# Performance work log

Measured on AMD Instinct MI355X. Metric: run time of the kernel, lower is better.

## Reference

```python
import jax, jax.numpy as jnp
import numpy as np

B, S, HID = 4, 4096, 768
NH, HD = 12, 64
KF = NH * HD          # 768, == HID
TTT_H = 2048
CS = 512              # chunk_size
NC = S // CS
LR = 0.001


def setup_inputs() -> dict:
    key = jax.random.key(0)
    ks = jax.random.split(key, 6)
    std = 0.02
    return {
        "x": jax.random.normal(ks[0], (B, S, HID), dtype=jnp.float32),
        "w_qkv": jax.random.normal(ks[1], (HID, 3 * HID), dtype=jnp.float32) * std,
        "w0": jax.random.normal(ks[2], (KF, TTT_H), dtype=jnp.float32) * std,
        "w1": jax.random.normal(ks[3], (TTT_H, HID), dtype=jnp.float32) * std,
        "w2": jax.random.normal(ks[4], (KF, TTT_H), dtype=jnp.float32) * std,
        "w_out": jax.random.normal(ks[5], (HID, HID), dtype=jnp.float32) * std,
    }


def _fast_forward(w0, w1, w2, k_in):
    # k_in: [B, CS, KF] -> [B, CS, HID]; SwiGLU-style fast-weight MLP
    gate = jax.nn.silu(k_in @ w0)
    hidden = k_in @ w2
    return (gate * hidden) @ w1


def reference(x, w_qkv, w0, w1, w2, w_out):
    qkv = x @ w_qkv                                   # [B,S,3*HID]
    q, k, v = jnp.split(qkv, 3, axis=-1)
    q = q.reshape(B, S, NH, HD)
    k = k.reshape(B, S, NH, HD)
    v = v.reshape(B, S, NH, HD)

    def step(carry, chunk_idx):
        w0c, w1c, w2c = carry
        start = chunk_idx * CS
        kc = jax.lax.dynamic_slice(k, (0, start, 0, 0), (B, CS, NH, HD)).reshape(B, CS, KF)
        vc = jax.lax.dynamic_slice(v, (0, start, 0, 0), (B, CS, NH, HD)).reshape(B, CS, KF)

        def loss_fn(a0, a1, a2):
            v_pred = _fast_forward(a0, a1, a2, kc)
            return jnp.mean((v_pred - vc) ** 2)

        loss, (g0, g1, g2) = jax.value_and_grad(loss_fn, argnums=(0, 1, 2))(w0c, w1c, w2c)
        w0n = w0c - LR * g0
        w1n = w1c - LR * g1
        w2n = w2c - LR * g2
        out = _fast_forward(w0n, w1n, w2n, kc)        # [B,CS,KF]
        return (w0n, w1n, w2n), (out, loss)

    _, (chunk_outs, chunk_losses) = jax.lax.scan(step, (w0, w1, w2), jnp.arange(NC))
    # [NC,B,CS,KF] -> [B,S,NH,HD]  (== concatenate chunks along seq axis)
    ttt = jnp.transpose(chunk_outs, (1, 0, 2, 3)).reshape(B, S, NH, HD)
    ttt = (q * ttt).reshape(B, S, HID)
    output = (x + ttt) @ w_out
    return output, jnp.mean(chunk_losses)
```

## Files before the change

### kernel.cpp

```cpp
#include <hip/hip_runtime.h>
#include <hip/hip_bf16.h>


#define DEVI __device__ __forceinline__

typedef unsigned short u16;
typedef unsigned char u8;
typedef __attribute__((ext_vector_type(8))) short bf16x8;
typedef __attribute__((ext_vector_type(4))) float f32x4;
typedef __attribute__((ext_vector_type(16))) float f32x16;
typedef __attribute__((ext_vector_type(4))) int i32x4;
typedef __attribute__((ext_vector_type(8))) int i32x8;

DEVI u16 f2b(float f) {
  __hip_bfloat16 h = __float2bfloat16(f);
  return *reinterpret_cast<u16*>(&h);
}
DEVI float b2f(u16 u) {
  __hip_bfloat16 h = *reinterpret_cast<__hip_bfloat16*>(&u);
  return __bfloat162float(h);
}
DEVI float silu_f(float z) { return z / (1.f + __expf(-z)); }
DEVI u8 f2f8(float f) {
  int p = __builtin_amdgcn_cvt_pk_fp8_f32(f, f, 0, false);
  return (u8)(p & 0xff);
}

typedef const __attribute__((address_space(1))) void* gas_ptr;
typedef __attribute__((address_space(3))) void* las_ptr;
DEVI void async_cp16(const void* g, void* l) {
  __builtin_amdgcn_global_load_lds((gas_ptr)g, (las_ptr)l, 16, 0, 0);
}


__global__ __launch_bounds__(256) void prep_all(
    const float* __restrict__ x, const float* __restrict__ w_qkv,
    const float* __restrict__ w0, const float* __restrict__ w2,
    const float* __restrict__ w1, const float* __restrict__ w_out,
    u16* __restrict__ xb, u16* __restrict__ wqkvT, u8* __restrict__ w02T8,
    u16* __restrict__ w1T, u16* __restrict__ woutT) {
  __shared__ float tile[32][33];
  const int tx = threadIdx.x, ty = threadIdx.y;
  const int bid = blockIdx.x;

  if (bid < 2048) {
    const int tid = ty * 32 + tx;
    const int n4 = 16384 * 768 / 4;
    for (int i = bid * 256 + tid; i < n4; i += 2048 * 256) {
      float4 f = reinterpret_cast<const float4*>(x)[i];
      uint2 u;
      u.x = (unsigned)f2b(f.x) | ((unsigned)f2b(f.y) << 16);
      u.y = (unsigned)f2b(f.z) | ((unsigned)f2b(f.w) << 16);
      reinterpret_cast<uint2*>(xb)[i] = u;
    }
    return;
  }

  const float* in;
  u16* out = nullptr;
  int R, C, mode, lid;
  if (bid < 3776)      { in = w_qkv; out = wqkvT; R = 768;  C = 2304; mode = 0; lid = bid - 2048; }
  else if (bid < 5312) { in = w0;    R = 768;  C = 2048; mode = 1; lid = bid - 3776; }
  else if (bid < 6848) { in = w2;    R = 768;  C = 2048; mode = 2; lid = bid - 5312; }
  else if (bid < 8384) { in = w1;    out = w1T;   R = 2048; C = 768;  mode = 0; lid = bid - 6848; }
  else                 { in = w_out; out = woutT; R = 768;  C = 768;  mode = 0; lid = bid - 8384; }
  const int nbx = C >> 5;
  const int c0 = (lid % nbx) * 32, r0 = (lid / nbx) * 32;
#pragma unroll
  for (int j = 0; j < 4; ++j)
    tile[ty + j * 8][tx] = in[(size_t)(r0 + ty + j * 8) * C + c0 + tx];
  __syncthreads();
#pragma unroll
  for (int j = 0; j < 4; ++j) {
    int c = c0 + ty + j * 8;
    int r = r0 + tx;
    float v = tile[tx][ty + j * 8];
    if (mode == 0) {
      out[(size_t)c * R + r] = f2b(v);
    } else {
      int orow = ((c >> 5) << 6) + ((mode == 2) ? 32 : 0) + (c & 31);
      w02T8[(size_t)orow * 768 + r] = f2f8(v);
    }
  }
}


template <typename Epi>
__global__ __launch_bounds__(512, 2) void gemm_mx(
    const u8* __restrict__ A, const u8* __restrict__ B, int K, Epi epi) {
  __shared__ __align__(16) u8 lds[3][32768];

  const int tid = threadIdx.x;
  const int lane = tid & 63;
  const int wave = tid >> 6;
  const int wm = wave >> 2;
  const int wn = wave & 3;

  const int bid = blockIdx.x;
  const int xcd = bid & 7, sub = bid >> 3;
  const int mg = (xcd >> 1) * 4 + ((sub >> 3) & 3);
  const int nti = (xcd & 1) * 8 + (sub & 7);
  const int n0 = nti * 256;

  const int srw = tid & 255;
  const int g0 = tid >> 8;

  const u8* Bsrc = B + (size_t)(n0 + srw) * K;
  u8* ldsb = &lds[0][0];

  auto stageA = [&](int buf, const u8* At, int kt) {
    const u8* src = At + kt * 64 + g0 * 16;
    u8* dst = ldsb + buf * 32768 + tid * 16;
    async_cp16(src, dst);
    async_cp16(src + 32, dst + 8192);
  };
  auto stageB = [&](int buf, int kt) {
    const u8* src = Bsrc + kt * 64 + g0 * 16;
    u8* dst = ldsb + buf * 32768 + 16384 + tid * 16;
    async_cp16(src, dst);
    async_cp16(src + 32, dst + 8192);
  };

  const int r32 = lane & 31;
  const int kh = lane >> 5;
  const int nt = K >> 6;
  const int total = nt * 4;

  const u8* At0 = A + ((size_t)(mg * 4) * 256 + srw) * K;
  const size_t tstride = (size_t)256 * K;

  stageA(0, At0, 0); stageB(0, 0);
  stageA(1, At0, 1); stageB(1, 1);
  asm volatile("s_waitcnt vmcnt(4)" ::: "memory");
  __builtin_amdgcn_s_barrier();
  asm volatile("" ::: "memory");

  f32x16 acc[4][2];
#pragma unroll
  for (int mt = 0; mt < 4; ++mt)
#pragma unroll
    for (int nq = 0; nq < 2; ++nq)
#pragma unroll
      for (int e = 0; e < 16; ++e) acc[mt][nq][e] = 0.f;

  const u8* Ast = At0;
  int kt_n = 2;
  int b = 0;
  int cur_tile = 0, kt_c = 0;

  for (int S = 0; S < total; ++S) {
    const u8* Ab = ldsb + b * 32768 + kh * 8192;
    const u8* Bb = Ab + 16384;

    i32x8 af[4], bfr[2];
#pragma unroll
    for (int mt = 0; mt < 4; ++mt) {
      const u8* p = Ab + (wm * 128 + mt * 32 + r32) * 16;
      i32x4 lo = *reinterpret_cast<const i32x4*>(p);
      i32x4 hi = *reinterpret_cast<const i32x4*>(p + 4096);
      af[mt][0] = lo[0]; af[mt][1] = lo[1]; af[mt][2] = lo[2]; af[mt][3] = lo[3];
      af[mt][4] = hi[0]; af[mt][5] = hi[1]; af[mt][6] = hi[2]; af[mt][7] = hi[3];
    }
#pragma unroll
    for (int nq = 0; nq < 2; ++nq) {
      const u8* p = Bb + (wn * 64 + nq * 32 + r32) * 16;
      i32x4 lo = *reinterpret_cast<const i32x4*>(p);
      i32x4 hi = *reinterpret_cast<const i32x4*>(p + 4096);
      bfr[nq][0] = lo[0]; bfr[nq][1] = lo[1]; bfr[nq][2] = lo[2]; bfr[nq][3] = lo[3];
      bfr[nq][4] = hi[0]; bfr[nq][5] = hi[1]; bfr[nq][6] = hi[2]; bfr[nq][7] = hi[3];
    }

    if (S + 2 < total) {
      int b2 = b + 2; if (b2 >= 3) b2 -= 3;
      stageA(b2, Ast, kt_n);
      stageB(b2, kt_n);
      ++kt_n; if (kt_n == nt) { kt_n = 0; Ast += tstride; }
    }

    __builtin_amdgcn_s_setprio(1);
#pragma unroll
    for (int mt = 0; mt < 4; ++mt)
#pragma unroll
      for (int nq = 0; nq < 2; ++nq)
        acc[mt][nq] = __builtin_amdgcn_mfma_scale_f32_32x32x64_f8f6f4(
            af[mt], bfr[nq], acc[mt][nq], 0, 0,
            0, 0x7F7F7F7F, 0, 0x7F7F7F7F);
    __builtin_amdgcn_s_setprio(0);
    asm volatile("" ::: "memory");

    if (S + 2 < total) {
      asm volatile("s_waitcnt vmcnt(4)" ::: "memory");
    } else if (S + 1 < total) {
      asm volatile("s_waitcnt vmcnt(0)" ::: "memory");
    }
    __builtin_amdgcn_s_barrier();
    asm volatile("" ::: "memory");

    if (++kt_c == nt) {
      epi(acc, (mg * 4 + cur_tile) * 256, n0, wm, wn, lane);
      kt_c = 0; ++cur_tile;
#pragma unroll
      for (int mt = 0; mt < 4; ++mt)
#pragma unroll
        for (int nq = 0; nq < 2; ++nq)
#pragma unroll
          for (int e = 0; e < 16; ++e) acc[mt][nq][e] = 0.f;
    }
    ++b; if (b == 3) b = 0;
  }
}

struct EpiGH32 {
  u16* gh;
  __device__ void operator()(f32x16 (&acc)[4][2], int m0, int n0, int wm,
                             int wn, int lane) const {
    const int r32 = lane & 31, kh = lane >> 5;
    const int colb = ((n0 + wn * 64) >> 1) + r32;
#pragma unroll
    for (int mt = 0; mt < 4; ++mt)
#pragma unroll
      for (int reg = 0; reg < 16; ++reg) {
        int row = m0 + wm * 128 + mt * 32 + (reg & 3) + 8 * (reg >> 2) + 4 * kh;
        float z = acc[mt][0][reg];
        float h = acc[mt][1][reg];
        gh[(size_t)row * 2048 + colb] = f2b(silu_f(z) * h);
      }
  }
};


template <typename Epi>
__global__ __launch_bounds__(256, 3) void gemm128(
    const u16* __restrict__ A, const u16* __restrict__ B,
    int M, int N, int K, int nbx, Epi epi) {
  __shared__ __align__(16) u16 As[3][128 * 32];
  __shared__ __align__(16) u16 Bs[3][128 * 32];

  const int t = threadIdx.x;
  const int lane = t & 63;
  const int wave = t >> 6;
  const int wm = wave >> 1;
  const int wn = wave & 1;
  const int cpx = gridDim.x >> 3;
  const int lid = (blockIdx.x & 7) * cpx + (blockIdx.x >> 3);
  const int m0 = (lid / nbx) * 128;
  const int n0 = (lid % nbx) * 128;

  const int sr = t >> 2;
  const int sg = (t & 3) ^ (sr & 3);
  unsigned aoff[2], boff[2];
#pragma unroll
  for (int i = 0; i < 2; ++i) {
    int r = sr + i * 64;
    aoff[i] = (unsigned)(m0 + r) * (unsigned)K + (unsigned)(sg * 8);
    boff[i] = (unsigned)(n0 + r) * (unsigned)K + (unsigned)(sg * 8);
  }

  const int rlo = lane & 15;
  const int kq = lane >> 4;

  f32x4 acc[4][4] = {};

  auto stage = [&](int b, int kt) {
#pragma unroll
    for (int i = 0; i < 2; ++i)
      async_cp16(A + (size_t)aoff[i] + kt, &As[b][0] + (t + i * 256) * 8);
#pragma unroll
    for (int i = 0; i < 2; ++i)
      async_cp16(B + (size_t)boff[i] + kt, &Bs[b][0] + (t + i * 256) * 8);
  };

  const int nt = K >> 5;
  stage(0, 0);
  stage(1, 32);
  asm volatile("s_waitcnt vmcnt(4)" ::: "memory");
  __builtin_amdgcn_s_barrier();
  asm volatile("" ::: "memory");

  int b = 0;
  for (int s = 0; s < nt; ++s) {
    bf16x8 af[4], bfv[4];
    const u16* ab = &As[b][0];
    const u16* bb = &Bs[b][0];
#pragma unroll
    for (int fm = 0; fm < 4; ++fm) {
      int r = wm * 64 + fm * 16 + rlo;
      int cc = kq ^ (r & 3);
      af[fm] = *reinterpret_cast<const bf16x8*>(ab + r * 32 + cc * 8);
    }
#pragma unroll
    for (int fn = 0; fn < 4; ++fn) {
      int r = wn * 64 + fn * 16 + rlo;
      int cc = kq ^ (r & 3);
      bfv[fn] = *reinterpret_cast<const bf16x8*>(bb + r * 32 + cc * 8);
    }
    __builtin_amdgcn_s_setprio(1);
#pragma unroll
    for (int fm = 0; fm < 4; ++fm)
#pragma unroll
      for (int fn = 0; fn < 4; ++fn)
        acc[fm][fn] = __builtin_amdgcn_mfma_f32_16x16x32_bf16(
            af[fm], bfv[fn], acc[fm][fn], 0, 0, 0);
    __builtin_amdgcn_s_setprio(0);
    asm volatile("" ::: "memory");

    if (s + 2 < nt) {
      int b2 = b + 2; if (b2 >= 3) b2 -= 3;
      stage(b2, (s + 2) << 5);
      asm volatile("s_waitcnt vmcnt(4)" ::: "memory");
      __builtin_amdgcn_s_barrier();
    } else if (s + 1 < nt) {
      asm volatile("s_waitcnt vmcnt(0)" ::: "memory");
      __builtin_amdgcn_s_barrier();
    }
    asm volatile("" ::: "memory");
    b = (b == 2) ? 0 : b + 1;
  }

  epi(acc, m0, n0, wm, wn, lane);
}

struct EpiQKV128 {
  u16 *q, *v;
  u8* k8;
  __device__ void operator()(f32x4 (&acc)[4][4], int m0, int n0, int wm, int wn, int lane) const {
    int third = n0 / 768;
    int nb = n0 - third * 768;
#pragma unroll
    for (int mi = 0; mi < 4; ++mi)
#pragma unroll
      for (int ni = 0; ni < 4; ++ni)
#pragma unroll
        for (int r = 0; r < 4; ++r) {
          int row = m0 + wm * 64 + mi * 16 + (lane >> 4) * 4 + r;
          int col = nb + wn * 64 + ni * 16 + (lane & 15);
          size_t idx = (size_t)row * 768 + col;
          float val = acc[mi][ni][r];
          if (third == 1) k8[idx] = f2f8(val);
          else if (third == 0) q[idx] = f2b(val);
          else v[idx] = f2b(val);
        }
  }
};

struct EpiC {
  const u16 *qb, *vb, *xb;
  u16* ub;
  float* lossp;
  __device__ void operator()(f32x4 (&acc)[4][4], int m0, int n0, int wm, int wn, int lane) const {
    float sq = 0.f;
#pragma unroll
    for (int mi = 0; mi < 4; ++mi)
#pragma unroll
      for (int ni = 0; ni < 4; ++ni)
#pragma unroll
        for (int r = 0; r < 4; ++r) {
          int row = m0 + wm * 64 + mi * 16 + (lane >> 4) * 4 + r;
          int col = n0 + wn * 64 + ni * 16 + (lane & 15);
          size_t idx = (size_t)row * 768 + col;
          float P = acc[mi][ni][r];
          float e = P - b2f(vb[idx]);
          sq += e * e;
          float u = b2f(xb[idx]) + b2f(qb[idx]) * P;
          ub[idx] = f2b(u);
        }
#pragma unroll
    for (int off = 32; off > 0; off >>= 1) sq += __shfl_down(sq, off, 64);
    __shared__ float red[4];
    int t = threadIdx.x;
    if ((t & 63) == 0) red[t >> 6] = sq;
    __syncthreads();
    if (t == 0) lossp[(m0 >> 7) * 6 + (n0 >> 7)] = red[0] + red[1] + red[2] + red[3];
  }
};

struct EpiD {
  float* out;
  const float* lossp;
  float* lossdst;
  __device__ void operator()(f32x4 (&acc)[4][4], int m0, int n0, int wm, int wn, int lane) const {
#pragma unroll
    for (int mi = 0; mi < 4; ++mi)
#pragma unroll
      for (int ni = 0; ni < 4; ++ni)
#pragma unroll
        for (int r = 0; r < 4; ++r) {
          int row = m0 + wm * 64 + mi * 16 + (lane >> 4) * 4 + r;
          int col = n0 + wn * 64 + ni * 16 + (lane & 15);
          out[(size_t)row * 768 + col] = acc[mi][ni][r];
        }
    if (blockIdx.x == 0) {
      int t = threadIdx.x;
      float s = lossp[t] + lossp[t + 256] + lossp[t + 512];
#pragma unroll
      for (int off = 32; off > 0; off >>= 1) s += __shfl_down(s, off, 64);
      __shared__ float red[4];
      if ((t & 63) == 0) red[t >> 6] = s;
      __syncthreads();
      if (t == 0) lossdst[0] = (red[0] + red[1] + red[2] + red[3]) * (1.f / 12582912.f);
    }
  }
};


extern "C" void kernel_launch(void* const* d_in, const int* in_sizes, int n_in,
                              void* d_out, int out_size, void* d_ws, size_t ws_size,
                              hipStream_t stream) {
  const float* x     = (const float*)d_in[0];
  const float* w_qkv = (const float*)d_in[1];
  const float* w0    = (const float*)d_in[2];
  const float* w1    = (const float*)d_in[3];
  const float* w2    = (const float*)d_in[4];
  const float* w_out = (const float*)d_in[5];
  float* out = (float*)d_out;

  const int M = 16384;
  char* ws = (char*)d_ws;
  size_t off = 0;
  auto alloc = [&](size_t bytes) {
    void* p = ws + off;
    off += (bytes + 255) & ~(size_t)255;
    return p;
  };
  u16* xb    = (u16*)alloc((size_t)M * 768 * 2);
  u16* qb    = (u16*)alloc((size_t)M * 768 * 2);
  u8*  kb8   = (u8*) alloc((size_t)M * 768);
  u16* vb    = (u16*)alloc((size_t)M * 768 * 2);
  u16* gh    = (u16*)alloc((size_t)M * 2048 * 2);
  u16* wqkvT = (u16*)alloc((size_t)2304 * 768 * 2);
  u8*  w02T8 = (u8*) alloc((size_t)4096 * 768);
  u16* w1T   = (u16*)alloc((size_t)768 * 2048 * 2);
  u16* woutT = (u16*)alloc((size_t)768 * 768 * 2);
  float* lossp = (float*)alloc(768 * 4);
  u16* ub = xb;

  prep_all<<<8960, dim3(32, 8), 0, stream>>>(
      x, w_qkv, w0, w2, w1, w_out, xb, wqkvT, w02T8, w1T, woutT);

  gemm128<<<dim3(128 * 18), 256, 0, stream>>>(
      xb, wqkvT, M, 2304, 768, 18, EpiQKV128{qb, vb, kb8});
  gemm_mx<<<dim3(256), 512, 0, stream>>>(
      kb8, w02T8, 768, EpiGH32{gh});
  gemm128<<<dim3(6 * 128), 256, 0, stream>>>(
      gh, w1T, M, 768, 2048, 6, EpiC{qb, vb, xb, ub, lossp});
  gemm128<<<dim3(6 * 128), 256, 0, stream>>>(
      ub, woutT, M, 768, 768, 6, EpiD{out, lossp, out + (size_t)M * 768});
}
```

Measured before the change: 303.3 us.

## Move gated-hidden GEMM to FP8 and replace persistent MX kernel with 128-tile FP8 GEMM

The w1 weights are now transposed into FP8, and the SwiGLU hidden activations are written as FP8 instead of bf16. The third GEMM (gh @ w1) now runs on the FP8 scaled MFMA path, which halves its operand traffic and raises MFMA throughput. The persistent 512-thread MX kernel for the k@w0/w2 GEMM is replaced by a generic non-persistent 128x128 FP8 GEMM with triple-buffered async LDS loads, used for both GEMMs. The cost is lower precision on the hidden activations and w1, which may loosen accuracy against the reference.

```diff
diff --git a/kernel.cpp b/kernel.cpp
--- a/kernel.cpp
+++ b/kernel.cpp
@@ -38,7 +38,7 @@
     const float* __restrict__ w0, const float* __restrict__ w2,
     const float* __restrict__ w1, const float* __restrict__ w_out,
     u16* __restrict__ xb, u16* __restrict__ wqkvT, u8* __restrict__ w02T8,
-    u16* __restrict__ w1T, u16* __restrict__ woutT) {
+    u8* __restrict__ w1T8, u16* __restrict__ woutT) {
   __shared__ float tile[32][33];
   const int tx = threadIdx.x, ty = threadIdx.y;
   const int bid = blockIdx.x;
@@ -62,7 +62,7 @@
   if (bid < 3776)      { in = w_qkv; out = wqkvT; R = 768;  C = 2304; mode = 0; lid = bid - 2048; }
   else if (bid < 5312) { in = w0;    R = 768;  C = 2048; mode = 1; lid = bid - 3776; }
   else if (bid < 6848) { in = w2;    R = 768;  C = 2048; mode = 2; lid = bid - 5312; }
-  else if (bid < 8384) { in = w1;    out = w1T;   R = 2048; C = 768;  mode = 0; lid = bid - 6848; }
+  else if (bid < 8384) { in = w1;    R = 2048; C = 768;  mode = 3; lid = bid - 6848; }
   else                 { in = w_out; out = woutT; R = 768;  C = 768;  mode = 0; lid = bid - 8384; }
   const int nbx = C >> 5;
   const int c0 = (lid % nbx) * 32, r0 = (lid / nbx) * 32;
@@ -77,6 +77,8 @@
     float v = tile[tx][ty + j * 8];
     if (mode == 0) {
       out[(size_t)c * R + r] = f2b(v);
+    } else if (mode == 3) {
+      w1T8[(size_t)c * R + r] = f2f8(v);
     } else {
       int orow = ((c >> 5) << 6) + ((mode == 2) ? 32 : 0) + (c & 31);
       w02T8[(size_t)orow * 768 + r] = f2f8(v);
@@ -86,155 +88,11 @@
 
 
 template <typename Epi>
-__global__ __launch_bounds__(512, 2) void gemm_mx(
-    const u8* __restrict__ A, const u8* __restrict__ B, int K, Epi epi) {
-  __shared__ __align__(16) u8 lds[3][32768];
-
-  const int tid = threadIdx.x;
-  const int lane = tid & 63;
-  const int wave = tid >> 6;
-  const int wm = wave >> 2;
-  const int wn = wave & 3;
-
-  const int bid = blockIdx.x;
-  const int xcd = bid & 7, sub = bid >> 3;
-  const int mg = (xcd >> 1) * 4 + ((sub >> 3) & 3);
-  const int nti = (xcd & 1) * 8 + (sub & 7);
-  const int n0 = nti * 256;
-
-  const int srw = tid & 255;
-  const int g0 = tid >> 8;
-
-  const u8* Bsrc = B + (size_t)(n0 + srw) * K;
-  u8* ldsb = &lds[0][0];
-
-  auto stageA = [&](int buf, const u8* At, int kt) {
-    const u8* src = At + kt * 64 + g0 * 16;
-    u8* dst = ldsb + buf * 32768 + tid * 16;
-    async_cp16(src, dst);
-    async_cp16(src + 32, dst + 8192);
-  };
-  auto stageB = [&](int buf, int kt) {
-    const u8* src = Bsrc + kt * 64 + g0 * 16;
-    u8* dst = ldsb + buf * 32768 + 16384 + tid * 16;
-    async_cp16(src, dst);
-    async_cp16(src + 32, dst + 8192);
-  };
-
-  const int r32 = lane & 31;
-  const int kh = lane >> 5;
-  const int nt = K >> 6;
-  const int total = nt * 4;
-
-  const u8* At0 = A + ((size_t)(mg * 4) * 256 + srw) * K;
-  const size_t tstride = (size_t)256 * K;
-
-  stageA(0, At0, 0); stageB(0, 0);
-  stageA(1, At0, 1); stageB(1, 1);
-  asm volatile("s_waitcnt vmcnt(4)" ::: "memory");
-  __builtin_amdgcn_s_barrier();
-  asm volatile("" ::: "memory");
-
-  f32x16 acc[4][2];
-#pragma unroll
-  for (int mt = 0; mt < 4; ++mt)
-#pragma unroll
-    for (int nq = 0; nq < 2; ++nq)
-#pragma unroll
-      for (int e = 0; e < 16; ++e) acc[mt][nq][e] = 0.f;
-
-  const u8* Ast = At0;
-  int kt_n = 2;
-  int b = 0;
-  int cur_tile = 0, kt_c = 0;
-
-  for (int S = 0; S < total; ++S) {
-    const u8* Ab = ldsb + b * 32768 + kh * 8192;
-    const u8* Bb = Ab + 16384;
-
-    i32x8 af[4], bfr[2];
-#pragma unroll
-    for (int mt = 0; mt < 4; ++mt) {
-      const u8* p = Ab + (wm * 128 + mt * 32 + r32) * 16;
-      i32x4 lo = *reinterpret_cast<const i32x4*>(p);
-      i32x4 hi = *reinterpret_cast<const i32x4*>(p + 4096);
-      af[mt][0] = lo[0]; af[mt][1] = lo[1]; af[mt][2] = lo[2]; af[mt][3] = lo[3];
-      af[mt][4] = hi[0]; af[mt][5] = hi[1]; af[mt][6] = hi[2]; af[mt][7] = hi[3];
-    }
-#pragma unroll
-    for (int nq = 0; nq < 2; ++nq) {
-      const u8* p = Bb + (wn * 64 + nq * 32 + r32) * 16;
-      i32x4 lo = *reinterpret_cast<const i32x4*>(p);
-      i32x4 hi = *reinterpret_cast<const i32x4*>(p + 4096);
-      bfr[nq][0] = lo[0]; bfr[nq][1] = lo[1]; bfr[nq][2] = lo[2]; bfr[nq][3] = lo[3];
-      bfr[nq][4] = hi[0]; bfr[nq][5] = hi[1]; bfr[nq][6] = hi[2]; bfr[nq][7] = hi[3];
-    }
-
-    if (S + 2 < total) {
-      int b2 = b + 2; if (b2 >= 3) b2 -= 3;
-      stageA(b2, Ast, kt_n);
-      stageB(b2, kt_n);
-      ++kt_n; if (kt_n == nt) { kt_n = 0; Ast += tstride; }
-    }
-
-    __builtin_amdgcn_s_setprio(1);
-#pragma unroll
-    for (int mt = 0; mt < 4; ++mt)
-#pragma unroll
-      for (int nq = 0; nq < 2; ++nq)
-        acc[mt][nq] = __builtin_amdgcn_mfma_scale_f32_32x32x64_f8f6f4(
-            af[mt], bfr[nq], acc[mt][nq], 0, 0,
-            0, 0x7F7F7F7F, 0, 0x7F7F7F7F);
-    __builtin_amdgcn_s_setprio(0);
-    asm volatile("" ::: "memory");
-
-    if (S + 2 < total) {
-      asm volatile("s_waitcnt vmcnt(4)" ::: "memory");
-    } else if (S + 1 < total) {
-      asm volatile("s_waitcnt vmcnt(0)" ::: "memory");
-    }
-    __builtin_amdgcn_s_barrier();
-    asm volatile("" ::: "memory");
-
-    if (++kt_c == nt) {
-      epi(acc, (mg * 4 + cur_tile) * 256, n0, wm, wn, lane);
-      kt_c = 0; ++cur_tile;
-#pragma unroll
-      for (int mt = 0; mt < 4; ++mt)
-#pragma unroll
-        for (int nq = 0; nq < 2; ++nq)
-#pragma unroll
-          for (int e = 0; e < 16; ++e) acc[mt][nq][e] = 0.f;
-    }
-    ++b; if (b == 3) b = 0;
-  }
-}
-
-struct EpiGH32 {
-  u16* gh;
-  __device__ void operator()(f32x16 (&acc)[4][2], int m0, int n0, int wm,
-                             int wn, int lane) const {
-    const int r32 = lane & 31, kh = lane >> 5;
-    const int colb = ((n0 + wn * 64) >> 1) + r32;
-#pragma unroll
-    for (int mt = 0; mt < 4; ++mt)
-#pragma unroll
-      for (int reg = 0; reg < 16; ++reg) {
-        int row = m0 + wm * 128 + mt * 32 + (reg & 3) + 8 * (reg >> 2) + 4 * kh;
-        float z = acc[mt][0][reg];
-        float h = acc[mt][1][reg];
-        gh[(size_t)row * 2048 + colb] = f2b(silu_f(z) * h);
-      }
-  }
-};
-
-
-template <typename Epi>
-__global__ __launch_bounds__(256, 3) void gemm128(
-    const u16* __restrict__ A, const u16* __restrict__ B,
-    int M, int N, int K, int nbx, Epi epi) {
-  __shared__ __align__(16) u16 As[3][128 * 32];
-  __shared__ __align__(16) u16 Bs[3][128 * 32];
+__global__ __launch_bounds__(256, 3) void gemm128f8(
+    const u8* __restrict__ A, const u8* __restrict__ B,
+    int K, int nbx, Epi epi) {
+  __shared__ __align__(16) u8 As[3][8192];
+  __shared__ __align__(16) u8 Bs[3][8192];
 
   const int t = threadIdx.x;
   const int lane = t & 63;
@@ -246,6 +104,150 @@
   const int m0 = (lid / nbx) * 128;
   const int n0 = (lid % nbx) * 128;
 
+  unsigned aoff[2], boff[2];
+#pragma unroll
+  for (int i = 0; i < 2; ++i) {
+    int s = t + i * 256;
+    int r = s & 127, g = s >> 7;
+    aoff[i] = (unsigned)(m0 + r) * (unsigned)K + (unsigned)(g * 16);
+    boff[i] = (unsigned)(n0 + r) * (unsigned)K + (unsigned)(g * 16);
+  }
+
+  const int r32 = lane & 31;
+  const int kh = lane >> 5;
+
+  f32x16 acc[2][2] = {};
+
+  auto stage = [&](int b, int kt) {
+#pragma unroll
+    for (int i = 0; i < 2; ++i)
+      async_cp16(A + (size_t)aoff[i] + kt, &As[b][0] + (t + i * 256) * 16);
+#pragma unroll
+    for (int i = 0; i < 2; ++i)
+      async_cp16(B + (size_t)boff[i] + kt, &Bs[b][0] + (t + i * 256) * 16);
+  };
+
+  const int nt = K >> 6;
+  stage(0, 0);
+  stage(1, 64);
+  asm volatile("s_waitcnt vmcnt(4)" ::: "memory");
+  __builtin_amdgcn_s_barrier();
+  asm volatile("" ::: "memory");
+
+  int b = 0;
+  for (int s = 0; s < nt; ++s) {
+    i32x8 af[2], bf[2];
+    const u8* ab = &As[b][0];
+    const u8* bb = &Bs[b][0];
+#pragma unroll
+    for (int mt = 0; mt < 2; ++mt) {
+      const u8* p = ab + (2 * kh) * 2048 + (wm * 64 + mt * 32 + r32) * 16;
+      i32x4 lo = *reinterpret_cast<const i32x4*>(p);
+      i32x4 hi = *reinterpret_cast<const i32x4*>(p + 2048);
+      af[mt] = __builtin_shufflevector(lo, hi, 0, 1, 2, 3, 4, 5, 6, 7);
+    }
+#pragma unroll
+    for (int nq = 0; nq < 2; ++nq) {
+      const u8* p = bb + (2 * kh) * 2048 + (wn * 64 + nq * 32 + r32) * 16;
+      i32x4 lo = *reinterpret_cast<const i32x4*>(p);
+      i32x4 hi = *reinterpret_cast<const i32x4*>(p + 2048);
+      bf[nq] = __builtin_shufflevector(lo, hi, 0, 1, 2, 3, 4, 5, 6, 7);
+    }
+    __builtin_amdgcn_s_setprio(1);
+#pragma unroll
+    for (int mt = 0; mt < 2; ++mt)
+#pragma unroll
+      for (int nq = 0; nq < 2; ++nq)
+        acc[mt][nq] = __builtin_amdgcn_mfma_scale_f32_32x32x64_f8f6f4(
+            af[mt], bf[nq], acc[mt][nq], 0, 0,
+            0, 0x7F7F7F7F, 0, 0x7F7F7F7F);
+    __builtin_amdgcn_s_setprio(0);
+    asm volatile("" ::: "memory");
+
+    if (s + 2 < nt) {
+      int b2 = b + 2; if (b2 >= 3) b2 -= 3;
+      stage(b2, (s + 2) << 6);
+      asm volatile("s_waitcnt vmcnt(4)" ::: "memory");
+      __builtin_amdgcn_s_barrier();
+    } else if (s + 1 < nt) {
+      asm volatile("s_waitcnt vmcnt(0)" ::: "memory");
+      __builtin_amdgcn_s_barrier();
+    }
+    asm volatile("" ::: "memory");
+    b = (b == 2) ? 0 : b + 1;
+  }
+
+  epi(acc, m0, n0, wm, wn, lane);
+}
+
+struct EpiGH8 {
+  u8* gh8;
+  __device__ void operator()(f32x16 (&acc)[2][2], int m0, int n0, int wm,
+                             int wn, int lane) const {
+    const int r32 = lane & 31, kh = lane >> 5;
+    const int col = ((n0 + wn * 64) >> 1) + r32;
+#pragma unroll
+    for (int mt = 0; mt < 2; ++mt)
+#pragma unroll
+      for (int reg = 0; reg < 16; ++reg) {
+        int row = m0 + wm * 64 + mt * 32 + (reg & 3) + 8 * (reg >> 2) + 4 * kh;
+        float z = acc[mt][0][reg];
+        float h = acc[mt][1][reg];
+        gh8[(size_t)row * 2048 + col] = f2f8(silu_f(z) * h);
+      }
+  }
+};
+
+struct EpiC32 {
+  const u16 *qb, *vb, *xb;
+  u16* ub;
+  float* lossp;
+  __device__ void operator()(f32x16 (&acc)[2][2], int m0, int n0, int wm,
+                             int wn, int lane) const {
+    const int r32 = lane & 31, kh = lane >> 5;
+    float sq = 0.f;
+#pragma unroll
+    for (int mt = 0; mt < 2; ++mt)
+#pragma unroll
+      for (int nq = 0; nq < 2; ++nq)
+#pragma unroll
+        for (int reg = 0; reg < 16; ++reg) {
+          int row = m0 + wm * 64 + mt * 32 + (reg & 3) + 8 * (reg >> 2) + 4 * kh;
+          int col = n0 + wn * 64 + nq * 32 + r32;
+          size_t idx = (size_t)row * 768 + col;
+          float P = acc[mt][nq][reg];
+          float e = P - b2f(vb[idx]);
+          sq += e * e;
+          ub[idx] = f2b(b2f(xb[idx]) + b2f(qb[idx]) * P);
+        }
+#pragma unroll
+    for (int off = 32; off > 0; off >>= 1) sq += __shfl_down(sq, off, 64);
+    __shared__ float red[4];
+    int t = threadIdx.x;
+    if ((t & 63) == 0) red[t >> 6] = sq;
+    __syncthreads();
+    if (t == 0) lossp[(m0 >> 7) * 6 + (n0 >> 7)] = red[0] + red[1] + red[2] + red[3];
+  }
+};
+
+
+template <typename Epi>
+__global__ __launch_bounds__(256, 3) void gemm128(
+    const u16* __restrict__ A, const u16* __restrict__ B,
+    int M, int N, int K, int nbx, Epi epi) {
+  __shared__ __align__(16) u16 As[3][128 * 32];
+  __shared__ __align__(16) u16 Bs[3][128 * 32];
+
+  const int t = threadIdx.x;
+  const int lane = t & 63;
+  const int wave = t >> 6;
+  const int wm = wave >> 1;
+  const int wn = wave & 1;
+  const int cpx = gridDim.x >> 3;
+  const int lid = (blockIdx.x & 7) * cpx + (blockIdx.x >> 3);
+  const int m0 = (lid / nbx) * 128;
+  const int n0 = (lid % nbx) * 128;
+
   const int sr = t >> 2;
   const int sg = (t & 3) ^ (sr & 3);
   unsigned aoff[2], boff[2];
@@ -340,37 +342,6 @@
           else if (third == 0) q[idx] = f2b(val);
           else v[idx] = f2b(val);
         }
-  }
-};
-
-struct EpiC {
-  const u16 *qb, *vb, *xb;
-  u16* ub;
-  float* lossp;
-  __device__ void operator()(f32x4 (&acc)[4][4], int m0, int n0, int wm, int wn, int lane) const {
-    float sq = 0.f;
-#pragma unroll
-    for (int mi = 0; mi < 4; ++mi)
-#pragma unroll
-      for (int ni = 0; ni < 4; ++ni)
-#pragma unroll
-        for (int r = 0; r < 4; ++r) {
-          int row = m0 + wm * 64 + mi * 16 + (lane >> 4) * 4 + r;
-          int col = n0 + wn * 64 + ni * 16 + (lane & 15);
-          size_t idx = (size_t)row * 768 + col;
-          float P = acc[mi][ni][r];
-          float e = P - b2f(vb[idx]);
-          sq += e * e;
-          float u = b2f(xb[idx]) + b2f(qb[idx]) * P;
-          ub[idx] = f2b(u);
-        }
-#pragma unroll
-    for (int off = 32; off > 0; off >>= 1) sq += __shfl_down(sq, off, 64);
-    __shared__ float red[4];
-    int t = threadIdx.x;
-    if ((t & 63) == 0) red[t >> 6] = sq;
-    __syncthreads();
-    if (t == 0) lossp[(m0 >> 7) * 6 + (n0 >> 7)] = red[0] + red[1] + red[2] + red[3];
   }
 };
 
@@ -426,23 +397,23 @@
   u16* qb    = (u16*)alloc((size_t)M * 768 * 2);
   u8*  kb8   = (u8*) alloc((size_t)M * 768);
   u16* vb    = (u16*)alloc((size_t)M * 768 * 2);
-  u16* gh    = (u16*)alloc((size_t)M * 2048 * 2);
+  u8*  gh8   = (u8*) alloc((size_t)M * 2048);
   u16* wqkvT = (u16*)alloc((size_t)2304 * 768 * 2);
   u8*  w02T8 = (u8*) alloc((size_t)4096 * 768);
-  u16* w1T   = (u16*)alloc((size_t)768 * 2048 * 2);
+  u8*  w1T8  = (u8*) alloc((size_t)768 * 2048);
   u16* woutT = (u16*)alloc((size_t)768 * 768 * 2);
   float* lossp = (float*)alloc(768 * 4);
   u16* ub = xb;
 
   prep_all<<<8960, dim3(32, 8), 0, stream>>>(
-      x, w_qkv, w0, w2, w1, w_out, xb, wqkvT, w02T8, w1T, woutT);
+      x, w_qkv, w0, w2, w1, w_out, xb, wqkvT, w02T8, w1T8, woutT);
 
   gemm128<<<dim3(128 * 18), 256, 0, stream>>>(
       xb, wqkvT, M, 2304, 768, 18, EpiQKV128{qb, vb, kb8});
-  gemm_mx<<<dim3(256), 512, 0, stream>>>(
-      kb8, w02T8, 768, EpiGH32{gh});
-  gemm128<<<dim3(6 * 128), 256, 0, stream>>>(
-      gh, w1T, M, 768, 2048, 6, EpiC{qb, vb, xb, ub, lossp});
+  gemm128f8<<<dim3(128 * 32), 256, 0, stream>>>(
+      kb8, w02T8, 768, 32, EpiGH8{gh8});
+  gemm128f8<<<dim3(6 * 128), 256, 0, stream>>>(
+      gh8, w1T8, 2048, 6, EpiC32{qb, vb, xb, ub, lossp});
   gemm128<<<dim3(6 * 128), 256, 0, stream>>>(
       ub, woutT, M, 768, 768, 6, EpiD{out, lossp, out + (size_t)M * 768});
 }
```

After: 344.2 us. 1.13x slower.

## Unroll fp8 GEMM k-loop by two with four LDS buffers and fewer barriers

Applied to the files above, without the earlier changes.

Processes two k-tiles per loop iteration using a four-deep LDS ring, staging two future tiles at once. One full vmcnt(0) wait and barrier now cover two k-steps instead of one. This is meant to cut synchronization overhead per MFMA step. The cost is more LDS (128KB) and a full memory drain at each barrier, which may expose load latency, and the loop now assumes the tile count is even.

```diff
diff --git a/kernel.cpp b/kernel.cpp
--- a/kernel.cpp
+++ b/kernel.cpp
@@ -30,6 +30,13 @@
 typedef __attribute__((address_space(3))) void* las_ptr;
 DEVI void async_cp16(const void* g, void* l) {
   __builtin_amdgcn_global_load_lds((gas_ptr)g, (las_ptr)l, 16, 0, 0);
+}
+
+DEVI i32x8 load_pair(const u8* p, int slab) {
+  i32x8 v;
+  *reinterpret_cast<i32x4*>(&v)       = *reinterpret_cast<const i32x4*>(p);
+  *(reinterpret_cast<i32x4*>(&v) + 1) = *reinterpret_cast<const i32x4*>(p + slab);
+  return v;
 }
 
 
@@ -88,7 +95,7 @@
 template <typename Epi>
 __global__ __launch_bounds__(512, 2) void gemm_mx(
     const u8* __restrict__ A, const u8* __restrict__ B, int K, Epi epi) {
-  __shared__ __align__(16) u8 lds[3][32768];
+  __shared__ __align__(16) u8 lds[4][32768];
 
   const int tid = threadIdx.x;
   const int lane = tid & 63;
@@ -131,7 +138,7 @@
 
   stageA(0, At0, 0); stageB(0, 0);
   stageA(1, At0, 1); stageB(1, 1);
-  asm volatile("s_waitcnt vmcnt(4)" ::: "memory");
+  asm volatile("s_waitcnt vmcnt(0)" ::: "memory");
   __builtin_amdgcn_s_barrier();
   asm volatile("" ::: "memory");
 
@@ -145,38 +152,51 @@
 
   const u8* Ast = At0;
   int kt_n = 2;
-  int b = 0;
   int cur_tile = 0, kt_c = 0;
 
-  for (int S = 0; S < total; ++S) {
-    const u8* Ab = ldsb + b * 32768 + kh * 8192;
-    const u8* Bb = Ab + 16384;
-
+  for (int S = 0; S < total; S += 2) {
+    const int b0 = S & 3, b1 = (S + 1) & 3;
     i32x8 af[4], bfr[2];
-#pragma unroll
-    for (int mt = 0; mt < 4; ++mt) {
-      const u8* p = Ab + (wm * 128 + mt * 32 + r32) * 16;
-      i32x4 lo = *reinterpret_cast<const i32x4*>(p);
-      i32x4 hi = *reinterpret_cast<const i32x4*>(p + 4096);
-      af[mt][0] = lo[0]; af[mt][1] = lo[1]; af[mt][2] = lo[2]; af[mt][3] = lo[3];
-      af[mt][4] = hi[0]; af[mt][5] = hi[1]; af[mt][6] = hi[2]; af[mt][7] = hi[3];
-    }
-#pragma unroll
-    for (int nq = 0; nq < 2; ++nq) {
-      const u8* p = Bb + (wn * 64 + nq * 32 + r32) * 16;
-      i32x4 lo = *reinterpret_cast<const i32x4*>(p);
-      i32x4 hi = *reinterpret_cast<const i32x4*>(p + 4096);
-      bfr[nq][0] = lo[0]; bfr[nq][1] = lo[1]; bfr[nq][2] = lo[2]; bfr[nq][3] = lo[3];
-      bfr[nq][4] = hi[0]; bfr[nq][5] = hi[1]; bfr[nq][6] = hi[2]; bfr[nq][7] = hi[3];
+
+    {
+      const u8* Ab = ldsb + b0 * 32768 + kh * 8192;
+      const u8* Bb = Ab + 16384;
+#pragma unroll
+      for (int mt = 0; mt < 4; ++mt)
+        af[mt] = load_pair(Ab + (wm * 128 + mt * 32 + r32) * 16, 4096);
+#pragma unroll
+      for (int nq = 0; nq < 2; ++nq)
+        bfr[nq] = load_pair(Bb + (wn * 64 + nq * 32 + r32) * 16, 4096);
     }
 
     if (S + 2 < total) {
-      int b2 = b + 2; if (b2 >= 3) b2 -= 3;
-      stageA(b2, Ast, kt_n);
-      stageB(b2, kt_n);
-      ++kt_n; if (kt_n == nt) { kt_n = 0; Ast += tstride; }
-    }
-
+      const int bs0 = (S + 2) & 3, bs1 = (S + 3) & 3;
+      stageA(bs0, Ast, kt_n);     stageB(bs0, kt_n);
+      stageA(bs1, Ast, kt_n + 1); stageB(bs1, kt_n + 1);
+      kt_n += 2;
+      if (kt_n == nt) { kt_n = 0; Ast += tstride; }
+    }
+
+    __builtin_amdgcn_s_setprio(1);
+#pragma unroll
+    for (int mt = 0; mt < 4; ++mt)
+#pragma unroll
+      for (int nq = 0; nq < 2; ++nq)
+        acc[mt][nq] = __builtin_amdgcn_mfma_scale_f32_32x32x64_f8f6f4(
+            af[mt], bfr[nq], acc[mt][nq], 0, 0,
+            0, 0x7F7F7F7F, 0, 0x7F7F7F7F);
+    __builtin_amdgcn_s_setprio(0);
+
+    {
+      const u8* Ab = ldsb + b1 * 32768 + kh * 8192;
+      const u8* Bb = Ab + 16384;
+#pragma unroll
+      for (int mt = 0; mt < 4; ++mt)
+        af[mt] = load_pair(Ab + (wm * 128 + mt * 32 + r32) * 16, 4096);
+#pragma unroll
+      for (int nq = 0; nq < 2; ++nq)
+        bfr[nq] = load_pair(Bb + (wn * 64 + nq * 32 + r32) * 16, 4096);
+    }
     __builtin_amdgcn_s_setprio(1);
 #pragma unroll
     for (int mt = 0; mt < 4; ++mt)
@@ -189,14 +209,13 @@
     asm volatile("" ::: "memory");
 
     if (S + 2 < total) {
-      asm volatile("s_waitcnt vmcnt(4)" ::: "memory");
-    } else if (S + 1 < total) {
       asm volatile("s_waitcnt vmcnt(0)" ::: "memory");
     }
     __builtin_amdgcn_s_barrier();
     asm volatile("" ::: "memory");
 
-    if (++kt_c == nt) {
+    kt_c += 2;
+    if (kt_c == nt) {
       epi(acc, (mg * 4 + cur_tile) * 256, n0, wm, wn, lane);
       kt_c = 0; ++cur_tile;
 #pragma unroll
@@ -206,7 +225,6 @@
 #pragma unroll
           for (int e = 0; e < 16; ++e) acc[mt][nq][e] = 0.f;
     }
-    ++b; if (b == 3) b = 0;
   }
 }
 
```

After: 319.0 us. +5.2%, slower.
